# Kernel optimization log

Hardware: AMD Instinct MI355X
Metric: run time of the kernel (lower is better)

The kernel has to match this reference:

```python
import jax, jax.numpy as jnp
import numpy as np

N, E, B = 100000, 500000, 64
H, C = 2, 128  # GAT heads, per-head channels
EPS = 1e-5


def _seg_mean(x, idx, n):
    s = jax.ops.segment_sum(x, idx, num_segments=n)
    cnt = jax.ops.segment_sum(jnp.ones((idx.shape[0],), x.dtype), idx, num_segments=n)
    cnt = jnp.maximum(cnt, 1.0)
    return s / cnt.reshape((n,) + (1,) * (x.ndim - 1))


def _bn(x, g, b):
    m = x.mean(0)
    v = x.var(0)  # biased, as torch BN uses for normalization
    return g * (x - m) / jnp.sqrt(v + EPS) + b


def _sage(x, src, dst, n, wl, wr, b):
    # PyG SAGEConv(mean): lin_l(mean_j x_j) + lin_r(x_i), bias on lin_l
    agg = _seg_mean(x[src], dst, n)
    return agg @ wl.T + x @ wr.T + b


def setup_inputs():
    key = jax.random.key(0)
    ks = jax.random.split(key, 24)
    w = lambda k, s: (jax.random.normal(k, s, jnp.float32) * 0.05)
    inp = {
        'pos': jax.random.normal(ks[0], (N, 3), jnp.float32),
        'edge_index': jax.random.randint(ks[1], (2, E), 0, N),
        'batch': jnp.sort(jax.random.randint(ks[2], (N,), 0, B)),
        # SAGEConv 1: 3 -> 128
        's1_wl': w(ks[3], (128, 3)), 's1_wr': w(ks[4], (128, 3)), 's1_b': jnp.zeros((128,), jnp.float32),
        # SAGEConv 2: 128 -> 128
        's2_wl': w(ks[5], (128, 128)), 's2_wr': w(ks[6], (128, 128)), 's2_b': jnp.zeros((128,), jnp.float32),
        # GATConv: 256 -> 128, heads=2, concat=False
        'g_w': w(ks[7], (H * C, 256)), 'g_asrc': w(ks[8], (H, C)), 'g_adst': w(ks[9], (H, C)), 'g_b': jnp.zeros((C,), jnp.float32),
        # decoder
        'd1_w': w(ks[10], (256, 128)), 'd1_b': jnp.zeros((256,), jnp.float32),
        'bn1_g': jnp.ones((256,), jnp.float32), 'bn1_b': jnp.zeros((256,), jnp.float32),
        'd2_w': w(ks[11], (128, 256)), 'd2_b': jnp.zeros((128,), jnp.float32),
        'bn2_g': jnp.ones((128,), jnp.float32), 'bn2_b': jnp.zeros((128,), jnp.float32),
        'd3_w': w(ks[12], (40, 128)), 'd3_b': jnp.zeros((40,), jnp.float32),
        'bn3_g': jnp.ones((40,), jnp.float32), 'bn3_b': jnp.zeros((40,), jnp.float32),
    }
    return inp


def reference(pos, edge_index, batch, s1_wl, s1_wr, s1_b, s2_wl, s2_wr, s2_b,
              g_w, g_asrc, g_adst, g_b, d1_w, d1_b, bn1_g, bn1_b,
              d2_w, d2_b, bn2_g, bn2_b, d3_w, d3_b, bn3_g, bn3_b):
    src, dst = edge_index[0], edge_index[1]

    x1 = jax.nn.relu(_sage(pos, src, dst, N, s1_wl, s1_wr, s1_b))
    x2 = jax.nn.relu(_sage(x1, src, dst, N, s2_wl, s2_wr, s2_b))
    x3 = jnp.concatenate([x1, x2], axis=-1)  # [N, 256]

    # GATConv with self-loops, dropout off (eval), aggr='mean'
    loop = jnp.arange(N, dtype=edge_index.dtype)
    src_sl = jnp.concatenate([src, loop])
    dst_sl = jnp.concatenate([dst, loop])
    xw = (x3 @ g_w.T).reshape(N, H, C)
    a_src = (xw * g_asrc).sum(-1)  # [N, H]
    a_dst = (xw * g_adst).sum(-1)
    e = jax.nn.leaky_relu(a_src[src_sl] + a_dst[dst_sl], 0.2)  # [E+N, H]
    e_max = jax.ops.segment_max(e, dst_sl, num_segments=N)
    e = jnp.exp(e - e_max[dst_sl])
    denom = jax.ops.segment_sum(e, dst_sl, num_segments=N)
    alpha = e / denom[dst_sl]
    msg = alpha[:, :, None] * xw[src_sl]  # [E+N, H, C]
    out = _seg_mean(msg, dst_sl, N)  # aggr='mean' over incoming edges
    x3 = out.mean(axis=1) + g_b  # average heads (concat=False) -> [N, 128]

    z = _seg_mean(x3, batch, B)  # global mean pool -> [B, 128]

    z = jax.nn.relu(_bn(z @ d1_w.T + d1_b, bn1_g, bn1_b))
    z = jax.nn.relu(_bn(z @ d2_w.T + d2_b, bn2_g, bn2_b))
    z = _bn(z @ d3_w.T + d3_b, bn3_g, bn3_b)
    return z, jnp.argmax(z, axis=-1)
```

## Files before the change

### kernel.cpp

```cpp
#include <hip/hip_runtime.h>
#include <math.h>

#define BN_EPS 1e-5f

typedef __attribute__((ext_vector_type(8))) short short8;
typedef __attribute__((ext_vector_type(4))) float f32x4;
typedef unsigned int uint_t;

__device__ __forceinline__ float bf2f(unsigned short u) {
  return __builtin_bit_cast(float, ((unsigned)u) << 16);
}
__device__ __forceinline__ unsigned short f2bf(float f) {
  unsigned u = __builtin_bit_cast(unsigned, f);
  unsigned r = (u + 0x7fffu + ((u >> 16) & 1u)) >> 16;
  return (unsigned short)r;
}
__device__ __forceinline__ uint_t packsplit(float x) {
  unsigned short h = f2bf(x);
  unsigned short l = f2bf(x - bf2f(h));
  return (uint_t)h | ((uint_t)l << 16);
}
__device__ __forceinline__ float unpk(uint_t u) {
  return bf2f((unsigned short)(u & 0xffffu)) + bf2f((unsigned short)(u >> 16));
}

__global__ void k_deg_sum1(const int* __restrict__ src, const int* __restrict__ dst,
                           const float* __restrict__ pos, int* __restrict__ deg,
                           float* __restrict__ sum1, int E) {
  int e = blockIdx.x * blockDim.x + threadIdx.x;
  if (e >= E) return;
  int s = src[e], d = dst[e];
  atomicAdd(&deg[d], 1);
  atomicAdd(&sum1[d * 3 + 0], pos[s * 3 + 0]);
  atomicAdd(&sum1[d * 3 + 1], pos[s * 3 + 1]);
  atomicAdd(&sum1[d * 3 + 2], pos[s * 3 + 2]);
}

__global__ void k_scan1(const int* __restrict__ deg, int* __restrict__ rowptr,
                        int* __restrict__ bsum, int N) {
  __shared__ int part[256];
  int t = threadIdx.x;
  int base = blockIdx.x * 1024;
  int v[4]; int s = 0;
#pragma unroll
  for (int i = 0; i < 4; i++) {
    int idx = base + t * 4 + i;
    v[i] = (idx < N) ? deg[idx] : 0;
    s += v[i];
  }
  part[t] = s;
  __syncthreads();
  for (int off = 1; off < 256; off <<= 1) {
    int x = (t >= off) ? part[t - off] : 0;
    __syncthreads();
    part[t] += x;
    __syncthreads();
  }
  int run = part[t] - s;
#pragma unroll
  for (int i = 0; i < 4; i++) {
    int idx = base + t * 4 + i;
    if (idx < N) rowptr[idx] = run;
    run += v[i];
  }
  if (t == 255) bsum[blockIdx.x] = part[255];
}

__global__ void k_scan2(int* __restrict__ bsum, int nb) {
  if (threadIdx.x == 0 && blockIdx.x == 0) {
    int run = 0;
    for (int i = 0; i < nb; i++) { int v = bsum[i]; bsum[i] = run; run += v; }
  }
}

__global__ void k_scan3(int* __restrict__ rowptr, const int* __restrict__ bsum,
                        int N, int E) {
  int i = blockIdx.x * blockDim.x + threadIdx.x;
  if (i < N) rowptr[i] += bsum[i >> 10];
  else if (i == N) rowptr[N] = E;
}

__global__ void k_fill(const int* __restrict__ src, const int* __restrict__ dst,
                       const int* __restrict__ rowptr, int* __restrict__ fill,
                       int* __restrict__ col, int E) {
  int e = blockIdx.x * blockDim.x + threadIdx.x;
  if (e >= E) return;
  int d = dst[e];
  int p = rowptr[d] + atomicAdd(&fill[d], 1);
  col[p] = src[e];
}

__global__ void k_sage1(const float* __restrict__ sum1, const int* __restrict__ deg,
                        const float* __restrict__ pos,
                        const float* __restrict__ wl, const float* __restrict__ wr,
                        const float* __restrict__ b,
                        uint_t* __restrict__ cat, int N) {
  int n = blockIdx.x;
  if (n >= N) return;
  int o = threadIdx.x;
  float c = fmaxf((float)deg[n], 1.f);
  float a0 = sum1[n * 3 + 0] / c, a1 = sum1[n * 3 + 1] / c, a2 = sum1[n * 3 + 2] / c;
  float p0 = pos[n * 3 + 0], p1 = pos[n * 3 + 1], p2 = pos[n * 3 + 2];
  float v = b[o] + wl[o * 3 + 0] * a0 + wl[o * 3 + 1] * a1 + wl[o * 3 + 2] * a2
                 + wr[o * 3 + 0] * p0 + wr[o * 3 + 1] * p1 + wr[o * 3 + 2] * p2;
  cat[(size_t)n * 256 + o] = packsplit(fmaxf(v, 0.f));
}

__global__ void k_agg_x1(const int* __restrict__ rowptr, const int* __restrict__ col,
                         const uint_t* __restrict__ cat,
                         uint_t* __restrict__ agg, int N) {
  int w = (blockIdx.x * blockDim.x + threadIdx.x) >> 6;
  int nw = (gridDim.x * blockDim.x) >> 6;
  int lane = threadIdx.x & 63;
  for (int n = w; n < N; n += nw) {
    int k0 = rowptr[n], k1 = rowptr[n + 1];
    float ax = 0.f, ay = 0.f;
    int k = k0;
    for (; k + 1 < k1; k += 2) {
      int s0 = col[k], s1 = col[k + 1];
      uint2 v0 = *(const uint2*)&cat[(size_t)s0 * 256 + lane * 2];
      uint2 v1 = *(const uint2*)&cat[(size_t)s1 * 256 + lane * 2];
      ax += unpk(v0.x) + unpk(v1.x);
      ay += unpk(v0.y) + unpk(v1.y);
    }
    if (k < k1) {
      int s = col[k];
      uint2 v = *(const uint2*)&cat[(size_t)s * 256 + lane * 2];
      ax += unpk(v.x);
      ay += unpk(v.y);
    }
    float inv = 1.f / fmaxf((float)(k1 - k0), 1.f);
    uint2 o;
    o.x = packsplit(ax * inv);
    o.y = packsplit(ay * inv);
    *(uint2*)&agg[(size_t)n * 128 + lane * 2] = o;
  }
}

__global__ void k_castcat(const float* __restrict__ a, const float* __restrict__ b,
                          unsigned short* __restrict__ oH, unsigned short* __restrict__ oL,
                          int K1, int K2, int M) {
  int i = blockIdx.x * blockDim.x + threadIdx.x;
  int K = K1 + K2;
  if (i >= M * K) return;
  int m = i / K, k = i - m * K;
  float v = (k < K1) ? a[m * K1 + k] : b[m * K2 + (k - K1)];
  unsigned short h = f2bf(v);
  oH[i] = h;
  oL[i] = f2bf(v - bf2f(h));
}

__global__ __launch_bounds__(256) void gemm_split(
    const uint_t* __restrict__ A1, int as1, int K1,
    const uint_t* __restrict__ A2, int as2,
    const unsigned short* __restrict__ WH, const unsigned short* __restrict__ WL,
    const float* __restrict__ bias,
    uint_t* __restrict__ C, int cs, int co, int Nr, int K, int relu,
    const float* __restrict__ asrc, const float* __restrict__ adst,
    float* __restrict__ attn) {
  __shared__ unsigned short smem[4 * 128 * 40];
  unsigned short (*AsH)[40] = (unsigned short (*)[40])smem;
  unsigned short (*AsL)[40] = (unsigned short (*)[40])(smem + 128 * 40);
  unsigned short (*BsH)[40] = (unsigned short (*)[40])(smem + 2 * 128 * 40);
  unsigned short (*BsL)[40] = (unsigned short (*)[40])(smem + 3 * 128 * 40);
  int tid = threadIdx.x;
  int bm = blockIdx.x, bn = blockIdx.y;
  int wv = tid >> 6, L = tid & 63;
  int m16 = L & 15, quad = L >> 4;
  int rbase = wv * 32;

  f32x4 acc[2][8];
#pragma unroll
  for (int i = 0; i < 2; i++)
#pragma unroll
    for (int j = 0; j < 8; j++) acc[i][j] = (f32x4){0.f, 0.f, 0.f, 0.f};

  for (int kt = 0; kt < K; kt += 32) {
    const uint_t* Ap;
    int ast, kl;
    if (kt < K1) { Ap = A1; ast = as1; kl = kt; }
    else         { Ap = A2; ast = as2; kl = kt - K1; }
#pragma unroll
    for (int i = 0; i < 2; i++) {
      int flat = tid * 2 + i;
      int row = flat >> 2;
      int kc = (flat & 3) * 8;
      int rg = bm * 128 + row;
      uint4 p0 = {0u, 0u, 0u, 0u}, p1 = {0u, 0u, 0u, 0u};
      if (rg < Nr) {
        const uint_t* ap = &Ap[(size_t)rg * ast + kl + kc];
        p0 = *(const uint4*)ap;
        p1 = *(const uint4*)(ap + 4);
      }
      uint_t h0 = (p0.x & 0xffffu) | (p0.y << 16), l0 = (p0.x >> 16) | (p0.y & 0xffff0000u);
      uint_t h1 = (p0.z & 0xffffu) | (p0.w << 16), l1 = (p0.z >> 16) | (p0.w & 0xffff0000u);
      uint_t h2 = (p1.x & 0xffffu) | (p1.y << 16), l2 = (p1.x >> 16) | (p1.y & 0xffff0000u);
      uint_t h3 = (p1.z & 0xffffu) | (p1.w << 16), l3 = (p1.z >> 16) | (p1.w & 0xffff0000u);
      *(uint4*)&AsH[row][kc] = make_uint4(h0, h1, h2, h3);
      *(uint4*)&AsL[row][kc] = make_uint4(l0, l1, l2, l3);
      int ng = bn * 128 + row;
      size_t wb = (size_t)ng * K + kt + kc;
      *(uint4*)&BsH[row][kc] = *(const uint4*)&WH[wb];
      *(uint4*)&BsL[row][kc] = *(const uint4*)&WL[wb];
    }
    __syncthreads();
    short8 afH[2], afL[2];
#pragma unroll
    for (int rt = 0; rt < 2; rt++) {
      afH[rt] = *(const short8*)&AsH[rbase + rt * 16 + m16][quad * 8];
      afL[rt] = *(const short8*)&AsL[rbase + rt * 16 + m16][quad * 8];
    }
#pragma unroll
    for (int ct = 0; ct < 8; ct++) {
      short8 bfH = *(const short8*)&BsH[ct * 16 + m16][quad * 8];
      short8 bfL = *(const short8*)&BsL[ct * 16 + m16][quad * 8];
#pragma unroll
      for (int rt = 0; rt < 2; rt++) {
        acc[rt][ct] = __builtin_amdgcn_mfma_f32_16x16x32_bf16(afH[rt], bfH, acc[rt][ct], 0, 0, 0);
        acc[rt][ct] = __builtin_amdgcn_mfma_f32_16x16x32_bf16(afH[rt], bfL, acc[rt][ct], 0, 0, 0);
        acc[rt][ct] = __builtin_amdgcn_mfma_f32_16x16x32_bf16(afL[rt], bfH, acc[rt][ct], 0, 0, 0);
      }
    }
    __syncthreads();
  }

  if (attn) {
#pragma unroll
    for (int rt = 0; rt < 2; rt++) {
#pragma unroll
      for (int r = 0; r < 4; r++) {
        float a = 0.f, d = 0.f;
#pragma unroll
        for (int ct = 0; ct < 8; ct++) {
          int cg = bn * 128 + ct * 16 + m16;
          float v = acc[rt][ct][r];
          a += v * asrc[cg];
          d += v * adst[cg];
        }
#pragma unroll
        for (int m = 8; m >= 1; m >>= 1) {
          a += __shfl_xor(a, m);
          d += __shfl_xor(d, m);
        }
        if (m16 == 0) {
          int rg = bm * 128 + rbase + rt * 16 + quad * 4 + r;
          if (rg < Nr) {
            attn[rg * 4 + bn] = a;
            attn[rg * 4 + 2 + bn] = d;
          }
        }
      }
    }
  }

  uint_t* T = (uint_t*)smem;
#pragma unroll
  for (int hc = 0; hc < 2; hc++) {
    if (hc) __syncthreads();
#pragma unroll
    for (int rt = 0; rt < 2; rt++) {
#pragma unroll
      for (int ctl = 0; ctl < 4; ctl++) {
        int ct = hc * 4 + ctl;
        int cg = bn * 128 + ct * 16 + m16;
        float bco = bias ? bias[cg] : 0.f;
#pragma unroll
        for (int r = 0; r < 4; r++) {
          int row = rbase + rt * 16 + quad * 4 + r;
          float v = acc[rt][ct][r] + bco;
          if (relu) v = fmaxf(v, 0.f);
          T[row * 65 + ctl * 16 + m16] = packsplit(v);
        }
      }
    }
    __syncthreads();
    int row = tid >> 1;
    int cb = (tid & 1) * 32;
    int rg = bm * 128 + row;
    if (rg < Nr) {
      size_t base = (size_t)rg * cs + co + bn * 128 + hc * 64 + cb;
#pragma unroll
      for (int i2 = 0; i2 < 8; i2++) {
        uint4 q = *(const uint4*)&T[row * 65 + cb + i2 * 4];
        *(uint4*)&C[base + i2 * 4] = q;
      }
    }
  }
}

__global__ void k_gat_gather(const int* __restrict__ rowptr, const int* __restrict__ col,
                             const uint_t* __restrict__ xw,
                             const float* __restrict__ attn,
                             const float* __restrict__ gb, float* __restrict__ x3g, int N) {
  int w = (blockIdx.x * blockDim.x + threadIdx.x) >> 6;
  int nw = (gridDim.x * blockDim.x) >> 6;
  int lane = threadIdx.x & 63;
  int h = lane >> 5;
  for (int n = w; n < N; n += nw) {
    int k0 = rowptr[n], k1 = rowptr[n + 1];
    float ad = attn[n * 4 + 2 + h];
    float a0 = 0.f, a1 = 0.f, a2 = 0.f, a3 = 0.f, den = 0.f;
    int k = k0;
    for (; k + 1 < k1; k += 2) {
      int s0 = col[k], s1 = col[k + 1];
      float e0 = attn[s0 * 4 + h] + ad;
      float e1 = attn[s1 * 4 + h] + ad;
      e0 = e0 >= 0.f ? e0 : 0.2f * e0;
      e1 = e1 >= 0.f ? e1 : 0.2f * e1;
      float w0 = expf(e0), w1 = expf(e1);
      uint4 x0 = *(const uint4*)&xw[(size_t)s0 * 256 + lane * 4];
      uint4 x1 = *(const uint4*)&xw[(size_t)s1 * 256 + lane * 4];
      a0 += w0 * unpk(x0.x) + w1 * unpk(x1.x);
      a1 += w0 * unpk(x0.y) + w1 * unpk(x1.y);
      a2 += w0 * unpk(x0.z) + w1 * unpk(x1.z);
      a3 += w0 * unpk(x0.w) + w1 * unpk(x1.w);
      den += w0 + w1;
    }
    if (k < k1) {
      int s = col[k];
      float ea = attn[s * 4 + h] + ad;
      float el = ea >= 0.f ? ea : 0.2f * ea;
      float wgt = expf(el);
      uint4 x = *(const uint4*)&xw[(size_t)s * 256 + lane * 4];
      a0 += wgt * unpk(x.x); a1 += wgt * unpk(x.y);
      a2 += wgt * unpk(x.z); a3 += wgt * unpk(x.w);
      den += wgt;
    }
    {
      float ea = attn[n * 4 + h] + ad;
      float el = ea >= 0.f ? ea : 0.2f * ea;
      float wgt = expf(el);
      uint4 x = *(const uint4*)&xw[(size_t)n * 256 + lane * 4];
      a0 += wgt * unpk(x.x); a1 += wgt * unpk(x.y);
      a2 += wgt * unpk(x.z); a3 += wgt * unpk(x.w);
      den += wgt;
    }
    float invD = 1.f / den;
    float q0 = a0 * invD, q1 = a1 * invD, q2 = a2 * invD, q3 = a3 * invD;
    float p0 = __shfl_xor(q0, 32), p1 = __shfl_xor(q1, 32);
    float p2 = __shfl_xor(q2, 32), p3 = __shfl_xor(q3, 32);
    if (lane < 32) {
      float invc = 1.f / (float)(k1 - k0 + 1);
      float4 g = *(const float4*)&gb[lane * 4];
      float4 r;
      r.x = 0.5f * (q0 + p0) * invc + g.x;
      r.y = 0.5f * (q1 + p1) * invc + g.y;
      r.z = 0.5f * (q2 + p2) * invc + g.z;
      r.w = 0.5f * (q3 + p3) * invc + g.w;
      *(float4*)&x3g[(size_t)n * 128 + lane * 4] = r;
    }
  }
}

__global__ void k_pool(const float* __restrict__ x3g, const int* __restrict__ batch,
                       float* __restrict__ zsum, float* __restrict__ zcnt, int N) {
  int t = threadIdx.x;
  int chunk = (N + gridDim.x - 1) / gridDim.x;
  int n0 = blockIdx.x * chunk;
  int n1 = min(N, n0 + chunk);
  if (n0 >= n1) return;
  int cur = batch[n0];
  float acc = 0.f, cacc = 0.f;
  for (int n = n0; n < n1; n++) {
    int b = batch[n];
    if (b != cur) {
      atomicAdd(&zsum[cur * 128 + t], acc);
      if (t == 0) atomicAdd(&zcnt[cur], cacc);
      acc = 0.f; cacc = 0.f; cur = b;
    }
    acc += x3g[(size_t)n * 128 + t];
    cacc += 1.f;
  }
  atomicAdd(&zsum[cur * 128 + t], acc);
  if (t == 0) atomicAdd(&zcnt[cur], cacc);
}

__global__ void dec_col(const float* __restrict__ X, float* __restrict__ Y,
                        const float* __restrict__ W, const float* __restrict__ bias,
                        const float* __restrict__ g, const float* __restrict__ beta,
                        int Ki, int Mo, int Bn, int relu,
                        const float* __restrict__ zcntp) {
  int m = blockIdx.x;
  int r = threadIdx.x;
  float dot = 0.f;
  const float* xr = &X[(size_t)r * Ki];
  const float* wr = &W[(size_t)m * Ki];
  for (int k = 0; k < Ki; k += 4) {
    float4 xv = *(const float4*)&xr[k];
    float4 wv = *(const float4*)&wr[k];
    dot += xv.x * wv.x + xv.y * wv.y + xv.z * wv.z + xv.w * wv.w;
  }
  if (zcntp) dot *= 1.f / fmaxf(zcntp[r], 1.f);
  float acc = dot + bias[m];
  float s = acc;
#pragma unroll
  for (int o = 32; o >= 1; o >>= 1) s += __shfl_xor(s, o);
  float mean = s / (float)Bn;
  float d = acc - mean;
  float v2 = d * d;
#pragma unroll
  for (int o = 32; o >= 1; o >>= 1) v2 += __shfl_xor(v2, o);
  float var = v2 / (float)Bn;
  float y = g[m] * d / sqrtf(var + BN_EPS) + beta[m];
  if (relu) y = fmaxf(y, 0.f);
  Y[(size_t)r * Mo + m] = y;
}

__global__ void k_argmax(const float* __restrict__ z, float* __restrict__ argout,
                         int Bn, int Mo) {
  int r = blockIdx.x * blockDim.x + threadIdx.x;
  if (r >= Bn) return;
  const float* yr = &z[(size_t)r * Mo];
  float best = yr[0];
  int bi = 0;
  for (int j = 1; j < Mo; j++)
    if (yr[j] > best) { best = yr[j]; bi = j; }
  argout[r] = (float)bi;
}

extern "C" void kernel_launch(void* const* d_in, const int* in_sizes, int n_in,
                              void* d_out, int out_size, void* d_ws, size_t ws_size,
                              hipStream_t stream) {
  const int N = in_sizes[0] / 3;
  const int E = in_sizes[1] / 2;
  const int Bn = out_size / 41;

  const float* pos = (const float*)d_in[0];
  const int* ei = (const int*)d_in[1];
  const int* src = ei;
  const int* dst = ei + E;
  const int* batch = (const int*)d_in[2];
  const float* s1_wl = (const float*)d_in[3];
  const float* s1_wr = (const float*)d_in[4];
  const float* s1_b  = (const float*)d_in[5];
  const float* s2_wl = (const float*)d_in[6];
  const float* s2_wr = (const float*)d_in[7];
  const float* s2_b  = (const float*)d_in[8];
  const float* g_w    = (const float*)d_in[9];
  const float* g_asrc = (const float*)d_in[10];
  const float* g_adst = (const float*)d_in[11];
  const float* g_b    = (const float*)d_in[12];
  const float* d1_w = (const float*)d_in[13];
  const float* d1_b = (const float*)d_in[14];
  const float* bn1_g = (const float*)d_in[15];
  const float* bn1_b = (const float*)d_in[16];
  const float* d2_w = (const float*)d_in[17];
  const float* d2_b = (const float*)d_in[18];
  const float* bn2_g = (const float*)d_in[19];
  const float* bn2_b = (const float*)d_in[20];
  const float* d3_w = (const float*)d_in[21];
  const float* d3_b = (const float*)d_in[22];
  const float* bn3_g = (const float*)d_in[23];
  const float* bn3_b = (const float*)d_in[24];

  size_t Ns = (size_t)N, Es = (size_t)E;
  char* p = (char*)d_ws;
  auto take = [&](size_t bytes) -> char* {
    char* r = p;
    p += (bytes + 255) & ~(size_t)255;
    return r;
  };
  int* deg    = (int*)take(Ns * 4);
  int* fillc  = (int*)take(Ns * 4);
  int* rowptr = (int*)take((Ns + 1) * 4);
  int* bsums  = (int*)take(1024);
  int* col    = (int*)take(Es * 4);
  float* sum1 = (float*)take(3 * Ns * 4);
  float* attn = (float*)take(4 * Ns * 4);
  uint_t* cat = (uint_t*)take(256 * Ns * 4);
  uint_t* agg = (uint_t*)take(128 * Ns * 4);
  uint_t* xw  = (uint_t*)take(256 * Ns * 4);
  unsigned short* wcH = (unsigned short*)take(128 * 256 * 2);
  unsigned short* wcL = (unsigned short*)take(128 * 256 * 2);
  unsigned short* gwH = (unsigned short*)take(256 * 256 * 2);
  unsigned short* gwL = (unsigned short*)take(256 * 256 * 2);
  float* zsum  = (float*)take(8192 * 4);
  float* zcnt  = (float*)take(256 * 4);
  float* db1   = (float*)take(16384 * 4);
  float* db2   = (float*)take(8192 * 4);
  float* x3g = (float*)agg;
  float* out = (float*)d_out;

  hipMemsetAsync(deg, 0, Ns * 4, stream);
  hipMemsetAsync(fillc, 0, Ns * 4, stream);
  hipMemsetAsync(sum1, 0, 3 * Ns * 4, stream);
  hipMemsetAsync(zsum, 0, 8192 * 4, stream);
  hipMemsetAsync(zcnt, 0, 256 * 4, stream);

  k_deg_sum1<<<(E + 255) / 256, 256, 0, stream>>>(src, dst, pos, deg, sum1, E);

  int nb = (N + 1023) / 1024;
  k_scan1<<<nb, 256, 0, stream>>>(deg, rowptr, bsums, N);
  k_scan2<<<1, 64, 0, stream>>>(bsums, nb);
  k_scan3<<<(N + 256) / 256, 256, 0, stream>>>(rowptr, bsums, N, E);
  k_fill<<<(E + 255) / 256, 256, 0, stream>>>(src, dst, rowptr, fillc, col, E);

  k_castcat<<<(128 * 256 + 255) / 256, 256, 0, stream>>>(s2_wl, s2_wr, wcH, wcL, 128, 128, 128);
  k_castcat<<<(256 * 256 + 255) / 256, 256, 0, stream>>>(g_w, nullptr, gwH, gwL, 256, 0, 256);

  k_sage1<<<N, 128, 0, stream>>>(sum1, deg, pos, s1_wl, s1_wr, s1_b, cat, N);
  k_agg_x1<<<2048, 256, 0, stream>>>(rowptr, col, cat, agg, N);

  dim3 g2((N + 127) / 128, 1);
  gemm_split<<<g2, 256, 0, stream>>>(agg, 128, 128, cat, 256,
                                     wcH, wcL, s2_b, cat, 256, 128, N, 256, 1,
                                     nullptr, nullptr, nullptr);

  dim3 g3((N + 127) / 128, 2);
  gemm_split<<<g3, 256, 0, stream>>>(cat, 256, 256, nullptr, 0,
                                     gwH, gwL, nullptr, xw, 256, 0, N, 256, 0,
                                     g_asrc, g_adst, attn);

  k_gat_gather<<<2048, 256, 0, stream>>>(rowptr, col, xw, attn, g_b, x3g, N);

  k_pool<<<2048, 128, 0, stream>>>(x3g, batch, zsum, zcnt, N);

  dec_col<<<256, Bn, 0, stream>>>(zsum, db1, d1_w, d1_b, bn1_g, bn1_b, 128, 256, Bn, 1, zcnt);
  dec_col<<<128, Bn, 0, stream>>>(db1, db2, d2_w, d2_b, bn2_g, bn2_b, 256, 128, Bn, 1, nullptr);
  dec_col<<<40, Bn, 0, stream>>>(db2, out, d3_w, d3_b, bn3_g, bn3_b, 128, 40, Bn, 0, nullptr);
  k_argmax<<<1, 64, 0, stream>>>(out, out + Bn * 40, Bn, 40);
}
```

Measured before the change: 639.8 us.

## Prefetch next GEMM tile into registers and unroll gather loops by four

The split-bf16 MFMA GEMM now loads the next K-tile from global memory into registers while the current tile's MFMAs run, then writes it to shared memory after the barrier. This hides global load latency behind compute. The SAGE aggregation and GAT gather loops are unrolled from two edges to four, so more independent row loads are in flight per wave. The cost is higher register pressure, which may lower occupancy, and a slightly different floating-point summation order.

Result: slower. 821.0 us (+28.3%).

```diff
diff --git a/kernel.cpp b/kernel.cpp
--- a/kernel.cpp
+++ b/kernel.cpp
@@ -116,14 +116,16 @@
     int k0 = rowptr[n], k1 = rowptr[n + 1];
     float ax = 0.f, ay = 0.f;
     int k = k0;
-    for (; k + 1 < k1; k += 2) {
-      int s0 = col[k], s1 = col[k + 1];
+    for (; k + 3 < k1; k += 4) {
+      int s0 = col[k], s1 = col[k + 1], s2 = col[k + 2], s3 = col[k + 3];
       uint2 v0 = *(const uint2*)&cat[(size_t)s0 * 256 + lane * 2];
       uint2 v1 = *(const uint2*)&cat[(size_t)s1 * 256 + lane * 2];
-      ax += unpk(v0.x) + unpk(v1.x);
-      ay += unpk(v0.y) + unpk(v1.y);
-    }
-    if (k < k1) {
+      uint2 v2 = *(const uint2*)&cat[(size_t)s2 * 256 + lane * 2];
+      uint2 v3 = *(const uint2*)&cat[(size_t)s3 * 256 + lane * 2];
+      ax += (unpk(v0.x) + unpk(v1.x)) + (unpk(v2.x) + unpk(v3.x));
+      ay += (unpk(v0.y) + unpk(v1.y)) + (unpk(v2.y) + unpk(v3.y));
+    }
+    for (; k < k1; k++) {
       int s = col[k];
       uint2 v = *(const uint2*)&cat[(size_t)s * 256 + lane * 2];
       ax += unpk(v.x);
@@ -169,40 +171,62 @@
   int m16 = L & 15, quad = L >> 4;
   int rbase = wv * 32;
 
-  f32x4 acc[2][8];
-#pragma unroll
-  for (int i = 0; i < 2; i++)
-#pragma unroll
-    for (int j = 0; j < 8; j++) acc[i][j] = (f32x4){0.f, 0.f, 0.f, 0.f};
-
-  for (int kt = 0; kt < K; kt += 32) {
+  int row_[2], kc_[2], rg_[2];
+  size_t wbase_[2];
+#pragma unroll
+  for (int i = 0; i < 2; i++) {
+    int flat = tid * 2 + i;
+    row_[i] = flat >> 2;
+    kc_[i] = (flat & 3) * 8;
+    rg_[i] = bm * 128 + row_[i];
+    wbase_[i] = (size_t)(bn * 128 + row_[i]) * K + kc_[i];
+  }
+
+  uint4 pa0[2], pa1[2], pbh[2], pbl[2];
+
+  auto load_tile = [&](int kt) {
     const uint_t* Ap;
     int ast, kl;
     if (kt < K1) { Ap = A1; ast = as1; kl = kt; }
     else         { Ap = A2; ast = as2; kl = kt - K1; }
 #pragma unroll
     for (int i = 0; i < 2; i++) {
-      int flat = tid * 2 + i;
-      int row = flat >> 2;
-      int kc = (flat & 3) * 8;
-      int rg = bm * 128 + row;
-      uint4 p0 = {0u, 0u, 0u, 0u}, p1 = {0u, 0u, 0u, 0u};
-      if (rg < Nr) {
-        const uint_t* ap = &Ap[(size_t)rg * ast + kl + kc];
-        p0 = *(const uint4*)ap;
-        p1 = *(const uint4*)(ap + 4);
+      uint4 z = {0u, 0u, 0u, 0u};
+      pa0[i] = z; pa1[i] = z;
+      if (rg_[i] < Nr) {
+        const uint_t* ap = &Ap[(size_t)rg_[i] * ast + kl + kc_[i]];
+        pa0[i] = *(const uint4*)ap;
+        pa1[i] = *(const uint4*)(ap + 4);
       }
+      pbh[i] = *(const uint4*)&WH[wbase_[i] + kt];
+      pbl[i] = *(const uint4*)&WL[wbase_[i] + kt];
+    }
+  };
+  auto store_tile = [&]() {
+#pragma unroll
+    for (int i = 0; i < 2; i++) {
+      uint4 p0 = pa0[i], p1 = pa1[i];
       uint_t h0 = (p0.x & 0xffffu) | (p0.y << 16), l0 = (p0.x >> 16) | (p0.y & 0xffff0000u);
       uint_t h1 = (p0.z & 0xffffu) | (p0.w << 16), l1 = (p0.z >> 16) | (p0.w & 0xffff0000u);
       uint_t h2 = (p1.x & 0xffffu) | (p1.y << 16), l2 = (p1.x >> 16) | (p1.y & 0xffff0000u);
       uint_t h3 = (p1.z & 0xffffu) | (p1.w << 16), l3 = (p1.z >> 16) | (p1.w & 0xffff0000u);
-      *(uint4*)&AsH[row][kc] = make_uint4(h0, h1, h2, h3);
-      *(uint4*)&AsL[row][kc] = make_uint4(l0, l1, l2, l3);
-      int ng = bn * 128 + row;
-      size_t wb = (size_t)ng * K + kt + kc;
-      *(uint4*)&BsH[row][kc] = *(const uint4*)&WH[wb];
-      *(uint4*)&BsL[row][kc] = *(const uint4*)&WL[wb];
-    }
+      *(uint4*)&AsH[row_[i]][kc_[i]] = make_uint4(h0, h1, h2, h3);
+      *(uint4*)&AsL[row_[i]][kc_[i]] = make_uint4(l0, l1, l2, l3);
+      *(uint4*)&BsH[row_[i]][kc_[i]] = pbh[i];
+      *(uint4*)&BsL[row_[i]][kc_[i]] = pbl[i];
+    }
+  };
+
+  f32x4 acc[2][8];
+#pragma unroll
+  for (int i = 0; i < 2; i++)
+#pragma unroll
+    for (int j = 0; j < 8; j++) acc[i][j] = (f32x4){0.f, 0.f, 0.f, 0.f};
+
+  load_tile(0);
+  store_tile();
+
+  for (int kt = 0; kt < K; kt += 32) {
     __syncthreads();
     short8 afH[2], afL[2];
 #pragma unroll
@@ -210,18 +234,25 @@
       afH[rt] = *(const short8*)&AsH[rbase + rt * 16 + m16][quad * 8];
       afL[rt] = *(const short8*)&AsL[rbase + rt * 16 + m16][quad * 8];
     }
+    short8 bH[8], bL[8];
 #pragma unroll
     for (int ct = 0; ct < 8; ct++) {
-      short8 bfH = *(const short8*)&BsH[ct * 16 + m16][quad * 8];
-      short8 bfL = *(const short8*)&BsL[ct * 16 + m16][quad * 8];
+      bH[ct] = *(const short8*)&BsH[ct * 16 + m16][quad * 8];
+      bL[ct] = *(const short8*)&BsL[ct * 16 + m16][quad * 8];
+    }
+    bool more = (kt + 32 < K);
+    if (more) load_tile(kt + 32);
+#pragma unroll
+    for (int ct = 0; ct < 8; ct++) {
 #pragma unroll
       for (int rt = 0; rt < 2; rt++) {
-        acc[rt][ct] = __builtin_amdgcn_mfma_f32_16x16x32_bf16(afH[rt], bfH, acc[rt][ct], 0, 0, 0);
-        acc[rt][ct] = __builtin_amdgcn_mfma_f32_16x16x32_bf16(afH[rt], bfL, acc[rt][ct], 0, 0, 0);
-        acc[rt][ct] = __builtin_amdgcn_mfma_f32_16x16x32_bf16(afL[rt], bfH, acc[rt][ct], 0, 0, 0);
+        acc[rt][ct] = __builtin_amdgcn_mfma_f32_16x16x32_bf16(afH[rt], bH[ct], acc[rt][ct], 0, 0, 0);
+        acc[rt][ct] = __builtin_amdgcn_mfma_f32_16x16x32_bf16(afH[rt], bL[ct], acc[rt][ct], 0, 0, 0);
+        acc[rt][ct] = __builtin_amdgcn_mfma_f32_16x16x32_bf16(afL[rt], bH[ct], acc[rt][ct], 0, 0, 0);
       }
     }
     __syncthreads();
+    if (more) store_tile();
   }
 
   if (attn) {
@@ -301,22 +332,26 @@
     float ad = attn[n * 4 + 2 + h];
     float a0 = 0.f, a1 = 0.f, a2 = 0.f, a3 = 0.f, den = 0.f;
     int k = k0;
-    for (; k + 1 < k1; k += 2) {
-      int s0 = col[k], s1 = col[k + 1];
-      float e0 = attn[s0 * 4 + h] + ad;
-      float e1 = attn[s1 * 4 + h] + ad;
+    for (; k + 3 < k1; k += 4) {
+      int s0 = col[k], s1 = col[k + 1], s2 = col[k + 2], s3 = col[k + 3];
+      float e0 = attn[s0 * 4 + h] + ad, e1 = attn[s1 * 4 + h] + ad;
+      float e2 = attn[s2 * 4 + h] + ad, e3 = attn[s3 * 4 + h] + ad;
       e0 = e0 >= 0.f ? e0 : 0.2f * e0;
       e1 = e1 >= 0.f ? e1 : 0.2f * e1;
-      float w0 = expf(e0), w1 = expf(e1);
+      e2 = e2 >= 0.f ? e2 : 0.2f * e2;
+      e3 = e3 >= 0.f ? e3 : 0.2f * e3;
+      float w0 = expf(e0), w1 = expf(e1), w2 = expf(e2), w3 = expf(e3);
       uint4 x0 = *(const uint4*)&xw[(size_t)s0 * 256 + lane * 4];
       uint4 x1 = *(const uint4*)&xw[(size_t)s1 * 256 + lane * 4];
-      a0 += w0 * unpk(x0.x) + w1 * unpk(x1.x);
-      a1 += w0 * unpk(x0.y) + w1 * unpk(x1.y);
-      a2 += w0 * unpk(x0.z) + w1 * unpk(x1.z);
-      a3 += w0 * unpk(x0.w) + w1 * unpk(x1.w);
-      den += w0 + w1;
-    }
-    if (k < k1) {
+      uint4 x2 = *(const uint4*)&xw[(size_t)s2 * 256 + lane * 4];
+      uint4 x3 = *(const uint4*)&xw[(size_t)s3 * 256 + lane * 4];
+      a0 += (w0 * unpk(x0.x) + w1 * unpk(x1.x)) + (w2 * unpk(x2.x) + w3 * unpk(x3.x));
+      a1 += (w0 * unpk(x0.y) + w1 * unpk(x1.y)) + (w2 * unpk(x2.y) + w3 * unpk(x3.y));
+      a2 += (w0 * unpk(x0.z) + w1 * unpk(x1.z)) + (w2 * unpk(x2.z) + w3 * unpk(x3.z));
+      a3 += (w0 * unpk(x0.w) + w1 * unpk(x1.w)) + (w2 * unpk(x2.w) + w3 * unpk(x3.w));
+      den += (w0 + w1) + (w2 + w3);
+    }
+    for (; k < k1; k++) {
       int s = col[k];
       float ea = attn[s * 4 + h] + ad;
       float el = ea >= 0.f ? ea : 0.2f * ea;
```
